# Kernel optimization log

Measured on AMD Instinct MI355X. Metric: run time of the kernel, lower is better.

Reference implementation:

```python
import jax, jax.numpy as jnp
import numpy as np

NUM_HEADS = 8
TAU = 0.5

@jax.custom_vjp
def spike(u):
    # Heaviside spike with rectangular surrogate gradient (width 1.0)
    return (u >= 0.0).astype(u.dtype)

def _spike_fwd(u):
    return spike(u), u

def _spike_bwd(u, g):
    return (g * (jnp.abs(u) < 0.5).astype(g.dtype),)

spike.defvjp(_spike_fwd, _spike_bwd)

def lif(x, thr=1.0):
    # Multi-step LIF over leading T axis: leaky integrate, fire, hard reset.
    def step(mem, xt):
        mem = mem * TAU + xt
        s = spike(mem - thr)
        return mem * (1.0 - s), s
    _, out = jax.lax.scan(step, jnp.zeros_like(x[0]), x)
    return out

def bn(x, g, b):
    # eval-mode BatchNorm over channel axis 2 (running_mean=0, running_var=1)
    shape = (1, 1, -1) + (1,) * (x.ndim - 3)
    return x * g.reshape(shape) + b.reshape(shape)

def ema_mems(q, alpha):
    # mems[0]=q[0]; mems[t]=alpha*mems[t-1]+(1-alpha)*q[t-1]
    def step(m, qp):
        m2 = alpha * m + (1.0 - alpha) * qp
        return m2, m2
    _, ms = jax.lax.scan(step, q[0], q[:-1])
    return jnp.concatenate([q[:1], ms], axis=0)

def setup_inputs() -> dict:
    key = jax.random.key(0)
    ks = jax.random.split(key, 16)
    T, B, C, H, W = 4, 16, 256, 32, 32
    Ch = 4 * C
    s = 0.05
    return {
        'x': jax.random.normal(ks[0], (T, B, C, H, W), jnp.float32),
        'q_w': jax.random.normal(ks[1], (C, C), jnp.float32) * s,
        'q_g': 1.0 + 0.02 * jax.random.normal(ks[2], (C,), jnp.float32),
        'q_b': 0.02 * jax.random.normal(ks[3], (C,), jnp.float32),
        'k_w': jax.random.normal(ks[4], (C, C), jnp.float32) * s,
        'k_g': 1.0 + 0.02 * jax.random.normal(ks[5], (C,), jnp.float32),
        'k_b': 0.02 * jax.random.normal(ks[6], (C,), jnp.float32),
        'proj_w': jax.random.normal(ks[7], (C, C), jnp.float32) * s,
        'proj_bias': 0.02 * jax.random.normal(ks[8], (C,), jnp.float32),
        'proj_g': 1.0 + 0.02 * jax.random.normal(ks[9], (C,), jnp.float32),
        'proj_b2': 0.02 * jax.random.normal(ks[10], (C,), jnp.float32),
        'mem_alpha': jnp.asarray(0.2, jnp.float32),
        'w1': jax.random.normal(ks[11], (Ch, C), jnp.float32) * s,
        'b1': 0.02 * jax.random.normal(ks[12], (Ch,), jnp.float32),
        'bn1_g': jnp.ones((Ch,), jnp.float32),
        'bn1_b': jnp.zeros((Ch,), jnp.float32),
        'w2': jax.random.normal(ks[13], (C, Ch), jnp.float32) * s,
        'b2': 0.02 * jax.random.normal(ks[14], (C,), jnp.float32),
        'bn2_g': jnp.ones((C,), jnp.float32),
        'bn2_b': jnp.zeros((C,), jnp.float32),
    }

def reference(x, q_w, q_g, q_b, k_w, k_g, k_b, proj_w, proj_bias, proj_g, proj_b2,
              mem_alpha, w1, b1, bn1_g, bn1_b, w2, b2, bn2_g, bn2_b):
    T, B, C, H, W = x.shape
    N = H * W
    h = NUM_HEADS
    d = C // h

    # ---- Token_QK_Attention ----
    xs = lif(x)                                   # [T,B,C,H,W] spikes
    xf = xs.reshape(T, B, C, N)
    q = lif(bn(jnp.einsum('tbcn,oc->tbon', xf, q_w), q_g, q_b))
    k = lif(bn(jnp.einsum('tbcn,oc->tbon', xf, k_w), k_g, k_b))
    q = q.reshape(T, B, h, d, N)
    k = k.reshape(T, B, h, d, N)
    mems = ema_mems(q, mem_alpha)                 # [T,B,h,d,N]
    # concat([mems,q], dim=3) then sum over dim 3 == sum(mems+q, dim 3)
    qsum = jnp.sum(mems + q, axis=3, keepdims=True)   # [T,B,h,1,N]
    attn = lif(qsum, thr=0.5)
    y = (attn * k).reshape(T, B, C, N)
    y = bn(jnp.einsum('tbcn,oc->tbon', y, proj_w) + proj_bias.reshape(1, 1, -1, 1),
           proj_g, proj_b2).reshape(T, B, C, H, W)
    x = x + y

    # ---- MLP (1x1 conv2d) ----
    z = lif(x)
    z = bn(jnp.einsum('tbchw,oc->tbohw', z, w1) + b1.reshape(1, 1, -1, 1, 1), bn1_g, bn1_b)
    z = lif(z)
    z = bn(jnp.einsum('tbchw,oc->tbohw', z, w2) + b2.reshape(1, 1, -1, 1, 1), bn2_g, bn2_b)
    return x + z
```

## Files before the change

### kernel.cpp

```cpp
#include <hip/hip_runtime.h>

typedef unsigned int u32;
typedef unsigned char u8;
typedef unsigned short u16;
typedef __attribute__((ext_vector_type(4))) u32 u32x4;
typedef __attribute__((ext_vector_type(4))) int i32x4;
typedef __attribute__((ext_vector_type(4))) float f32x4;

#define DEV __device__ __forceinline__

static constexpr size_t XS_OFF  = 0;
static constexpr size_t QS_OFF  = XS_OFF  + (size_t)16777216;
static constexpr size_t KS_OFF  = QS_OFF  + (size_t)16777216;
static constexpr size_t ATT_OFF = KS_OFF  + (size_t)16777216;
static constexpr size_t X2_OFF  = ATT_OFF + (size_t)1048576;
static constexpr size_t Z2_OFF  = X2_OFF  + (size_t)67108864;
static constexpr size_t WQK_OFF = Z2_OFF  + (size_t)67108864;
static constexpr size_t WP_OFF  = WQK_OFF + (size_t)524288;
static constexpr size_t W1_OFF  = WP_OFF  + (size_t)262144;
static constexpr size_t W2_OFF  = W1_OFF  + (size_t)1048576;
static constexpr size_t WS_NEED = W2_OFF  + (size_t)1048576;

DEV void gl_lds16(const void* gsrc, void* ldst){
  __builtin_amdgcn_global_load_lds(
      (const __attribute__((address_space(1))) unsigned int*)gsrc,
      (__attribute__((address_space(3))) unsigned int*)ldst, 16, 0, 0);
}

__global__ __launch_bounds__(256) void prep_w(const float* __restrict__ S, signed char* __restrict__ D,
                                              int O, int Ck, int OTs, int otbase)
{
  int tid = blockIdx.x*256 + threadIdx.x;
  int tot = (O*Ck) >> 4;
  if (tid >= tot) return;
  int lane = tid & 63; int fo = tid >> 6;
  int OT = O >> 4; int KT = Ck >> 6;
  int kt = fo / OT; int ot = fo - kt*OT;
  int o = (ot<<4) + (lane&15);
  int c = (kt<<6) + ((lane>>4)<<4);
  const float* sp = S + (size_t)o*Ck + c;
  u8 dg[4][16];
#pragma unroll
  for (int j=0;j<16;j++){
    double w = (double)sp[j];
    int Mhi = (int)__double2ll_rn(w * 32768.0);
    double r = w - (double)Mhi * (1.0/32768.0);
    int Mlo = (int)__double2ll_rn(r * 2147483648.0);
    if (Mlo > 32639){ Mhi += 1; Mlo -= 65536; }
    int d1 = (int)(signed char)(Mhi & 255); int d0 = (Mhi - d1) >> 8;
    int d3 = (int)(signed char)(Mlo & 255); int d2 = (Mlo - d3) >> 8;
    dg[0][j]=(u8)d0; dg[1][j]=(u8)d1; dg[2][j]=(u8)d2; dg[3][j]=(u8)d3;
  }
#pragma unroll
  for (int g=0; g<4; g++){
    signed char* dp = D + ((size_t)((g*KT + kt)*OTs + otbase + ot)<<10) + lane*16;
    *(u32x4*)dp = *(const u32x4*)dg[g];
  }
}

__global__ __launch_bounds__(256,4) void lif_x(const float* __restrict__ X, u8* __restrict__ XSo)
{
  int tid = blockIdx.x*256 + threadIdx.x;
  int n = tid & 1023; int oct = (tid>>10)&31; int b = tid>>15;
  int c0 = oct<<3;
  float mem[8];
#pragma unroll
  for (int i=0;i<8;i++) mem[i]=0.f;
#pragma unroll
  for (int t=0;t<4;t++){
    unsigned long long pk = 0ull;
    const float* xp = X + ((size_t)(((t*16+b)<<8) + c0)<<10) + n;
#pragma unroll
    for (int i=0;i<8;i++){
      float xv = xp[(size_t)i<<10];
      mem[i] = __fadd_rn(__fmul_rn(mem[i],0.5f), xv);
      bool s = mem[i] >= 1.0f;
      if (s) pk |= (1ull << (i*8));
      mem[i] = s? 0.f : mem[i];
    }
    *(unsigned long long*)(XSo + ((size_t)(((t*16+b)<<10) + n)<<8) + c0) = pk;
  }
}

DEV u32 nib4(u32 u){ return ((u & 0x01010101u) * 0x01020408u) >> 24; }
DEV u32 pk16(u32x4 v){ return nib4(v[0]) | (nib4(v[1])<<4) | (nib4(v[2])<<8) | (nib4(v[3])<<12); }

__global__ __launch_bounds__(256,4) void attn_k(const u8* __restrict__ QS, u8* __restrict__ ATT,
                                                const float* __restrict__ alpha_p)
{
  const int tid = threadIdx.x; const int l = tid & 63; const int wv = tid>>6;
  int wid = blockIdx.x*4 + wv;
  int b = wid >> 7; int nc = wid & 127; int n0 = nc<<3;
  int nr = (l>>3)&7; int ch8 = l&7;
  const float a = alpha_p[0]; const float oma = __fsub_rn(1.0f, a);
  u32 mk[4];
#pragma unroll
  for (int t=0;t<4;t++){
    const u32x4* p = (const u32x4*)(QS + ((size_t)(((t*16+b)<<10) + n0 + nr) << 8));
    u32x4 v0 = p[ch8]; u32x4 v1 = p[8+ch8];
    u32 pa = pk16(v0), pb = pk16(v1);
    u32 qa = __shfl_xor(pa, 1); u32 qb = __shfl_xor(pb, 1);
    mk[t] = (l&1)? (qb | (pb<<16)) : (pa | (qa<<16));
  }
  float mt1[2], mt2[4], mt3[8];
#pragma unroll
  for (int q0=0;q0<2;q0++){
    mt1[q0] = __fadd_rn(__fmul_rn(a,(float)q0), __fmul_rn(oma,(float)q0));
#pragma unroll
    for (int q1=0;q1<2;q1++){
      mt2[q0+(q1<<1)] = __fadd_rn(__fmul_rn(a,mt1[q0]), __fmul_rn(oma,(float)q1));
#pragma unroll
      for (int q2=0;q2<2;q2++)
        mt3[q0+(q1<<1)+(q2<<2)] = __fadd_rn(__fmul_rn(a,mt2[q0+(q1<<1)]), __fmul_rn(oma,(float)q2));
    }
  }
  const int h = ((l&7)>>1) + ((l&1)<<2);
  const int n = n0 + nr;
  float mem = 0.f;
#pragma unroll
  for (int t=0;t<4;t++){
    u32 act = mk[0];
    if (t>=1) act |= mk[1];
    if (t>=2) act |= mk[2];
    if (t>=3) act |= mk[3];
    float qsum = 0.f;
    while (act){
      int d = __builtin_ctz(act); act &= act-1;
      int b0 = (mk[0]>>d)&1;
      float m;
      if (t==0) m = (float)b0;
      else if (t==1) m = mt1[b0];
      else if (t==2) m = mt2[b0 + (((mk[1]>>d)&1)<<1)];
      else m = mt3[b0 + (((mk[1]>>d)&1)<<1) + (((mk[2]>>d)&1)<<2)];
      float qd = (float)((mk[t]>>d)&1);
      qsum = __fadd_rn(qsum, __fadd_rn(m, qd));
    }
    mem = __fadd_rn(__fmul_rn(mem, 0.5f), qsum);
    bool s = mem >= 0.5f;
    ATT[((size_t)(((t*16+b)<<3) + h)<<10) + n] = s? (u8)1 : (u8)0;
    mem = s? 0.f : mem;
  }
}

__global__ __launch_bounds__(256) void mask_k(const u8* __restrict__ KS,
                                              const u8* __restrict__ ATT, u8* __restrict__ YS)
{
  int tid = blockIdx.x*256 + threadIdx.x;
  int c4 = tid & 15; int n = (tid>>4) & 1023; int tb = tid >> 14;
  int h = c4 >> 1;
  u8 m = ATT[((size_t)((tb<<3) + h)<<10) + n];
  size_t row = ((size_t)((tb<<10)+n))<<8;
  u32x4 v = *(const u32x4*)(KS + row + c4*16);
  if (!m) v = (u32x4){0,0,0,0};
  *(u32x4*)(YS + row + c4*16) = v;
}

template<int MODE>
__global__ __launch_bounds__(256,2) void gemm_i8(
    const u8* __restrict__ A, const signed char* __restrict__ W,
    const float* __restrict__ G1, const float* __restrict__ B1,
    const float* __restrict__ G2, const float* __restrict__ B2,
    const float* __restrict__ BIAS, const float* __restrict__ XRES,
    float* __restrict__ FOUT, u8* __restrict__ SOUT, u8* __restrict__ SOUT2)
{
  constexpr int KC   = (MODE==3)? 1024 : 256;
  constexpr int KT   = KC >> 6;
  constexpr int OTOT = (MODE==0)? 32 : (MODE==2)? 64 : 16;
  constexpr int NOB  = OTOT >> 1;
  constexpr int NWG  = NOB*256;

  const int tid = threadIdx.x;
  const int bid = blockIdx.x;
  const int wid = (bid & 7)*(NWG>>3) + (bid>>3);
  const int ob = wid % NOB; const int rr = wid / NOB;
  const int nb = rr & 15; const int b = rr >> 4;

  __shared__ __align__(16) u8 Al[16384];
  __shared__ __align__(16) u8 Bl[8192];

  const int lane = tid & 63, wv = tid >> 6;

  const u8* aRowG = A + (size_t)(((wv*16 + b)<<10) + nb*64 + lane)*KC;
  u8* aDst = Al + (wv<<2)*1024;

  i32x4 acc[4][2][4];
#pragma unroll
  for (int g=0;g<4;g++)
#pragma unroll
    for (int os=0;os<2;os++)
#pragma unroll
      for (int t=0;t<4;t++) acc[g][os][t] = (i32x4){0,0,0,0};

  for (int kt=0; kt<KT; ++kt){
    __syncthreads();
    const u8* as = aRowG + kt*64;
#pragma unroll
    for (int c=0;c<4;c++) gl_lds16(as + c*16, aDst + c*1024);
#pragma unroll
    for (int q2=0;q2<2;q2++){
      int fi = wv*2 + q2;
      const signed char* bs = W + ((size_t)(((fi>>1)*KT + kt)*OTOT + ob*2 + (fi&1))<<10) + lane*16;
      gl_lds16(bs, Bl + (fi<<10));
    }
    __syncthreads();

    i32x4 af[4];
#pragma unroll
    for (int t=0;t<4;t++)
      af[t] = *(const i32x4*)(Al + (((t<<2) + (lane>>4))*64 + (wv<<4) + (lane&15))*16);
#pragma unroll
    for (int g=0; g<4; ++g)
#pragma unroll
      for (int os=0; os<2; ++os){
        i32x4 bf = *(const i32x4*)(Bl + (((g<<1)+os)<<10) + lane*16);
#pragma unroll
        for (int t=0;t<4;t++)
          acc[g][os][t] = __builtin_amdgcn_mfma_i32_16x16x64_i8(af[t], bf, acc[g][os][t], 0,0,0);
      }
  }

  const int g4 = lane >> 4;
  const int nq = nb*64 + (wv<<4) + (g4<<2);

  float pre[2][4][4];
#pragma unroll
  for (int os=0;os<2;++os)
#pragma unroll
    for (int t=0;t<4;++t)
#pragma unroll
      for (int jj=0;jj<4;++jj){
        int shi = (acc[0][os][t][jj] << 8) + acc[1][os][t][jj];
        int slo = (acc[2][os][t][jj] << 8) + acc[3][os][t][jj];
        pre[os][t][jj] = (float)((double)shi * 0x1p-15 + (double)slo * 0x1p-31);
      }

  if constexpr (MODE==0){
#pragma unroll
    for (int os=0; os<2; ++os){
      const int o = (ob<<5) + (os<<4) + (lane&15);
      const int matk = o>>8; const int om = o & 255;
      const float gg = (matk? G2 : G1)[om];
      const float bb = (matk? B2 : B1)[om];
      u8* sp = matk? SOUT2 : SOUT;
#pragma unroll
      for (int jj=0;jj<4;jj++){
        float mem = 0.f; const int n = nq + jj;
#pragma unroll
        for (int t=0;t<4;t++){
          float v = __fadd_rn(__fmul_rn(pre[os][t][jj], gg), bb);
          mem = __fadd_rn(__fmul_rn(mem, 0.5f), v);
          const bool s = mem >= 1.0f;
          sp[(size_t)(((t*16 + b)<<10) + n)*256 + om] = s? (u8)1 : (u8)0;
          mem = s? 0.f : mem;
        }
      }
    }
  } else if constexpr (MODE==1){
#pragma unroll
    for (int os=0; os<2; ++os){
      const int o = (ob<<5) + (os<<4) + (lane&15);
      const float pg = G1[o], pb2v = B1[o], pbv = BIAS[o];
      float xv[4][4];
#pragma unroll
      for (int t=0;t<4;t++){
        const size_t base = ((size_t)(((t*16 + b)<<8) + o)<<10) + nq;
        const f32x4 xq = *(const f32x4*)(XRES + base);
        f32x4 ov;
#pragma unroll
        for (int jj=0;jj<4;jj++){
          float y2 = __fadd_rn(__fmul_rn(__fadd_rn(pre[os][t][jj], pbv), pg), pb2v);
          float xx = __fadd_rn(xq[jj], y2);
          xv[t][jj] = xx; ov[jj] = xx;
        }
        *(f32x4*)(FOUT + base) = ov;
      }
#pragma unroll
      for (int jj=0;jj<4;jj++){
        float mem = 0.f; const int n = nq + jj;
#pragma unroll
        for (int t=0;t<4;t++){
          mem = __fadd_rn(__fmul_rn(mem, 0.5f), xv[t][jj]);
          const bool s = mem >= 1.0f;
          SOUT[(size_t)(((t*16 + b)<<10) + n)*256 + o] = s? (u8)1 : (u8)0;
          mem = s? 0.f : mem;
        }
      }
    }
  } else if constexpr (MODE==2){
#pragma unroll
    for (int os=0; os<2; ++os){
      const int o = (ob<<5) + (os<<4) + (lane&15);
      const float gg = G1[o], bb = B1[o], bv = BIAS[o];
#pragma unroll
      for (int jj=0;jj<4;jj++){
        float mem = 0.f; const int n = nq + jj;
#pragma unroll
        for (int t=0;t<4;t++){
          float v = __fadd_rn(__fmul_rn(__fadd_rn(pre[os][t][jj], bv), gg), bb);
          mem = __fadd_rn(__fmul_rn(mem, 0.5f), v);
          const bool s = mem >= 1.0f;
          SOUT[(size_t)(((t*16 + b)<<10) + n)*1024 + o] = s? (u8)1 : (u8)0;
          mem = s? 0.f : mem;
        }
      }
    }
  } else {
#pragma unroll
    for (int os=0; os<2; ++os){
      const int o = (ob<<5) + (os<<4) + (lane&15);
      const float gg = G1[o], bb = B1[o], bv = BIAS[o];
#pragma unroll
      for (int t=0;t<4;t++){
        const size_t base = ((size_t)(((t*16 + b)<<8) + o)<<10) + nq;
        const f32x4 xq = *(const f32x4*)(XRES + base);
        f32x4 ov;
#pragma unroll
        for (int jj=0;jj<4;jj++){
          float v = __fadd_rn(__fmul_rn(__fadd_rn(pre[os][t][jj], bv), gg), bb);
          ov[jj] = __fadd_rn(xq[jj], v);
        }
        *(f32x4*)(FOUT + base) = ov;
      }
    }
  }
}

extern "C" void kernel_launch(void* const* d_in, const int* in_sizes, int n_in,
                              void* d_out, int out_size, void* d_ws, size_t ws_size,
                              hipStream_t stream)
{
  (void)in_sizes; (void)n_in; (void)out_size;
  if (ws_size < WS_NEED) return;

  const float* x      = (const float*)d_in[0];
  const float* q_w    = (const float*)d_in[1];
  const float* q_g    = (const float*)d_in[2];
  const float* q_b    = (const float*)d_in[3];
  const float* k_w    = (const float*)d_in[4];
  const float* k_g    = (const float*)d_in[5];
  const float* k_b    = (const float*)d_in[6];
  const float* p_w    = (const float*)d_in[7];
  const float* p_bias = (const float*)d_in[8];
  const float* p_g    = (const float*)d_in[9];
  const float* p_b2   = (const float*)d_in[10];
  const float* alpha  = (const float*)d_in[11];
  const float* w1     = (const float*)d_in[12];
  const float* b1     = (const float*)d_in[13];
  const float* bn1g   = (const float*)d_in[14];
  const float* bn1b   = (const float*)d_in[15];
  const float* w2     = (const float*)d_in[16];
  const float* b2     = (const float*)d_in[17];
  const float* bn2g   = (const float*)d_in[18];
  const float* bn2b   = (const float*)d_in[19];

  u8* ws  = (u8*)d_ws;
  u8* XS  = ws + XS_OFF;
  u8* QS  = ws + QS_OFF;
  u8* KS  = ws + KS_OFF;
  u8* ATT = ws + ATT_OFF;
  float* X2 = (float*)(ws + X2_OFF);
  u8* Z2  = ws + Z2_OFF;
  u8* YS  = QS;
  u8* Z   = XS;
  signed char* WQK = (signed char*)(ws + WQK_OFF);
  signed char* WPp = (signed char*)(ws + WP_OFF);
  signed char* W1p = (signed char*)(ws + W1_OFF);
  signed char* W2p = (signed char*)(ws + W2_OFF);

  prep_w<<<16, 256, 0, stream>>>(q_w, WQK, 256, 256, 32, 0);
  prep_w<<<16, 256, 0, stream>>>(k_w, WQK, 256, 256, 32, 16);
  prep_w<<<16, 256, 0, stream>>>(p_w, WPp, 256, 256, 16, 0);
  prep_w<<<64, 256, 0, stream>>>(w1,  W1p, 1024, 256, 64, 0);
  prep_w<<<64, 256, 0, stream>>>(w2,  W2p, 256, 1024, 16, 0);

  lif_x<<<2048, 256, 0, stream>>>(x, XS);

  gemm_i8<0><<<4096, 256, 0, stream>>>(XS, WQK, q_g, q_b, k_g, k_b,
                                       nullptr, nullptr, nullptr, QS, KS);

  attn_k<<<512, 256, 0, stream>>>(QS, ATT, alpha);
  mask_k<<<4096, 256, 0, stream>>>(KS, ATT, YS);

  gemm_i8<1><<<2048, 256, 0, stream>>>(YS, WPp, p_g, p_b2, nullptr, nullptr,
                                       p_bias, x, X2, Z, nullptr);

  gemm_i8<2><<<8192, 256, 0, stream>>>(Z, W1p, bn1g, bn1b, nullptr, nullptr,
                                       b1, nullptr, nullptr, Z2, nullptr);

  gemm_i8<3><<<2048, 256, 0, stream>>>(Z2, W2p, bn2g, bn2b, nullptr, nullptr,
                                       b2, X2, (float*)d_out, nullptr, nullptr);
}
```

Measured before the change: 536.7 us.

## Double-buffer int8 GEMM LDS tiles, preload full B panel, fuse weight prep launches

After: 517.7 us. -3.5%, faster.

```diff
diff --git a/kernel.cpp b/kernel.cpp
--- a/kernel.cpp
+++ b/kernel.cpp
@@ -27,12 +27,21 @@
       (__attribute__((address_space(3))) unsigned int*)ldst, 16, 0, 0);
 }
 
-__global__ __launch_bounds__(256) void prep_w(const float* __restrict__ S, signed char* __restrict__ D,
-                                              int O, int Ck, int OTs, int otbase)
-{
-  int tid = blockIdx.x*256 + threadIdx.x;
-  int tot = (O*Ck) >> 4;
-  if (tid >= tot) return;
+__global__ __launch_bounds__(256) void prep_all(
+    const float* __restrict__ q_w, const float* __restrict__ k_w,
+    const float* __restrict__ p_w, const float* __restrict__ w1,
+    const float* __restrict__ w2,
+    signed char* __restrict__ WQK, signed char* __restrict__ WP,
+    signed char* __restrict__ W1p, signed char* __restrict__ W2p)
+{
+  const int bb = blockIdx.x;
+  const float* S; signed char* D; int O, Ck, OTs, otbase, base;
+  if      (bb < 16) { S=q_w; D=WQK; O=256;  Ck=256;  OTs=32; otbase=0;  base=0;   }
+  else if (bb < 32) { S=k_w; D=WQK; O=256;  Ck=256;  OTs=32; otbase=16; base=16;  }
+  else if (bb < 48) { S=p_w; D=WP;  O=256;  Ck=256;  OTs=16; otbase=0;  base=32;  }
+  else if (bb <112) { S=w1;  D=W1p; O=1024; Ck=256;  OTs=64; otbase=0;  base=48;  }
+  else              { S=w2;  D=W2p; O=256;  Ck=1024; OTs=16; otbase=0;  base=112; }
+  int tid = (bb - base)*256 + threadIdx.x;
   int lane = tid & 63; int fo = tid >> 6;
   int OT = O >> 4; int KT = Ck >> 6;
   int kt = fo / OT; int ot = fo - kt*OT;
@@ -168,6 +177,7 @@
   constexpr int OTOT = (MODE==0)? 32 : (MODE==2)? 64 : 16;
   constexpr int NOB  = OTOT >> 1;
   constexpr int NWG  = NOB*256;
+  constexpr bool BUP = (MODE != 3);
 
   const int tid = threadIdx.x;
   const int bid = blockIdx.x;
@@ -175,48 +185,84 @@
   const int ob = wid % NOB; const int rr = wid / NOB;
   const int nb = rr & 15; const int b = rr >> 4;
 
-  __shared__ __align__(16) u8 Al[16384];
-  __shared__ __align__(16) u8 Bl[8192];
+  __shared__ __align__(16) u8 Al[2][16384];
+  __shared__ __align__(16) u8 Bl[BUP ? 32768 : 16384];
 
   const int lane = tid & 63, wv = tid >> 6;
 
   const u8* aRowG = A + (size_t)(((wv*16 + b)<<10) + nb*64 + lane)*KC;
-  u8* aDst = Al + (wv<<2)*1024;
-
-  i32x4 acc[4][2][4];
-#pragma unroll
-  for (int g=0;g<4;g++)
-#pragma unroll
-    for (int os=0;os<2;os++)
-#pragma unroll
-      for (int t=0;t<4;t++) acc[g][os][t] = (i32x4){0,0,0,0};
-
-  for (int kt=0; kt<KT; ++kt){
-    __syncthreads();
+
+  auto stageA = [&](int kt, int p){
     const u8* as = aRowG + kt*64;
-#pragma unroll
-    for (int c=0;c<4;c++) gl_lds16(as + c*16, aDst + c*1024);
+    u8* ad = Al[p] + (wv<<2)*1024;
+#pragma unroll
+    for (int c=0;c<4;c++) gl_lds16(as + c*16, ad + c*1024);
+  };
+  auto stageB3 = [&](int kt, int p){
 #pragma unroll
     for (int q2=0;q2<2;q2++){
       int fi = wv*2 + q2;
       const signed char* bs = W + ((size_t)(((fi>>1)*KT + kt)*OTOT + ob*2 + (fi&1))<<10) + lane*16;
-      gl_lds16(bs, Bl + (fi<<10));
-    }
-    __syncthreads();
-
+      gl_lds16(bs, Bl + p*8192 + (fi<<10));
+    }
+  };
+
+  i32x4 acc[4][2][4];
+#pragma unroll
+  for (int g=0;g<4;g++)
+#pragma unroll
+    for (int os=0;os<2;os++)
+#pragma unroll
+      for (int t=0;t<4;t++) acc[g][os][t] = (i32x4){0,0,0,0};
+
+  if constexpr (BUP){
+#pragma unroll
+    for (int j=0;j<8;j++){
+      int f = wv + j*4;
+      int g = f >> 3; int os = (f>>2)&1; int kt = f&3;
+      const signed char* bs = W + ((size_t)((g*KT + kt)*OTOT + ob*2 + os)<<10) + lane*16;
+      gl_lds16(bs, Bl + (f<<10));
+    }
+  }
+  stageA(0, 0);
+  if constexpr (!BUP) stageB3(0, 0);
+
+  auto compute = [&](int p, int kt){
     i32x4 af[4];
 #pragma unroll
     for (int t=0;t<4;t++)
-      af[t] = *(const i32x4*)(Al + (((t<<2) + (lane>>4))*64 + (wv<<4) + (lane&15))*16);
+      af[t] = *(const i32x4*)(Al[p] + (((t<<2)+(lane>>4))<<10) + (((wv<<4)+(lane&15))<<4));
+    __builtin_amdgcn_s_setprio(1);
 #pragma unroll
     for (int g=0; g<4; ++g)
 #pragma unroll
       for (int os=0; os<2; ++os){
-        i32x4 bf = *(const i32x4*)(Bl + (((g<<1)+os)<<10) + lane*16);
+        const u8* bp;
+        if constexpr (BUP) bp = Bl + (((((g<<1)+os)<<2) | kt)<<10);
+        else               bp = Bl + p*8192 + ((((g<<1)+os))<<10);
+        i32x4 bf = *(const i32x4*)(bp + (lane<<4));
 #pragma unroll
         for (int t=0;t<4;t++)
           acc[g][os][t] = __builtin_amdgcn_mfma_i32_16x16x64_i8(af[t], bf, acc[g][os][t], 0,0,0);
       }
+    __builtin_amdgcn_s_setprio(0);
+  };
+
+#pragma unroll
+  for (int kt=0; kt<KT; ++kt){
+    const int p = kt & 1;
+    if (kt+1 < KT){
+      stageA(kt+1, p^1);
+      if constexpr (!BUP) stageB3(kt+1, p^1);
+      if constexpr (BUP) asm volatile("s_waitcnt vmcnt(4)" ::: "memory");
+      else               asm volatile("s_waitcnt vmcnt(6)" ::: "memory");
+    } else {
+      asm volatile("s_waitcnt vmcnt(0)" ::: "memory");
+    }
+    __builtin_amdgcn_s_barrier();
+    compute(p, kt);
+    asm volatile("s_waitcnt lgkmcnt(0)" ::: "memory");
+    __builtin_amdgcn_s_barrier();
   }
 
   const int g4 = lane >> 4;
@@ -367,11 +413,7 @@
   signed char* W1p = (signed char*)(ws + W1_OFF);
   signed char* W2p = (signed char*)(ws + W2_OFF);
 
-  prep_w<<<16, 256, 0, stream>>>(q_w, WQK, 256, 256, 32, 0);
-  prep_w<<<16, 256, 0, stream>>>(k_w, WQK, 256, 256, 32, 16);
-  prep_w<<<16, 256, 0, stream>>>(p_w, WPp, 256, 256, 16, 0);
-  prep_w<<<64, 256, 0, stream>>>(w1,  W1p, 1024, 256, 64, 0);
-  prep_w<<<64, 256, 0, stream>>>(w2,  W2p, 256, 1024, 16, 0);
+  prep_all<<<176, 256, 0, stream>>>(q_w, k_w, p_w, w1, w2, WQK, WPp, W1p, W2p);
 
   lif_x<<<2048, 256, 0, stream>>>(x, XS);
 
```
